# Optimization experiments

Measured on AMD Instinct MI355X. Metric: run time of the kernel, lower is better.

The kernel has to match this reference:

```python
import jax, jax.numpy as jnp
import numpy as np

IN_FEATURES = 4096
OUT_FEATURES = 4096
GROUP_SIZE = 128
N_GROUPS = IN_FEATURES // GROUP_SIZE
N_LEVELS = 16
SCALE = float(np.sqrt(GROUP_SIZE))


def setup_inputs() -> dict:
    key = jax.random.key(0)
    k_x, k_idx, k_cb, k_norm, k_rot = jax.random.split(key, 5)
    x = jax.random.normal(k_x, (4, 2048, IN_FEATURES), dtype=jnp.float32)
    # packed 4-bit indices: each uint8 byte holds two 4-bit codes (stored as int32 here)
    indices_packed = jax.random.randint(k_idx, (OUT_FEATURES, IN_FEATURES // 2), 0, 256, dtype=jnp.int32)
    codebook = jax.random.normal(k_cb, (N_LEVELS,), dtype=jnp.float32)
    weight_norms = jax.random.uniform(k_norm, (OUT_FEATURES, N_GROUPS), dtype=jnp.float32) + 0.5
    # per-group random orthogonal rotations (QR of gaussian), matching generate_rotation_matrix semantics
    g = jax.random.normal(k_rot, (N_GROUPS, GROUP_SIZE, GROUP_SIZE), dtype=jnp.float32)
    q, _ = jnp.linalg.qr(g)
    rotations = q.astype(jnp.float32)
    return {"x": x, "indices_packed": indices_packed, "codebook": codebook,
            "weight_norms": weight_norms, "rotations": rotations}


def _unpack_4bit(packed):
    # packed: (N, K//2) -> (N, K); even columns from low nibble, odd from high nibble
    low = packed & 0xF
    high = (packed >> 4) & 0xF
    return jnp.stack([low, high], axis=-1).reshape(packed.shape[0], -1)


def reference(x, indices_packed, codebook, weight_norms, rotations):
    B, S, K = x.shape
    xf = x.reshape(-1, K).astype(jnp.float32)            # (T, K)
    T = xf.shape[0]
    # group-wise rotation: x_rot_g = x_g @ Pi_g.T
    xg = xf.reshape(T, N_GROUPS, GROUP_SIZE)             # (T, G, g)
    x_rot = jnp.einsum('tgk,gjk->tgj', xg, rotations)    # (T, G, g)
    # dequantized codes (before norm scaling)
    idx = _unpack_4bit(indices_packed)                    # (N, K)
    W = codebook[idx].reshape(OUT_FEATURES, N_GROUPS, GROUP_SIZE)  # (N, G, g)
    # out[t,n] = sum_g (x_rot[t,g,:] . W[n,g,:]) * norms[n,g] / scale
    out = jnp.einsum('tgj,ngj,ng->tn', x_rot, W, weight_norms / SCALE)
    return out.reshape(B, S, OUT_FEATURES).astype(x.dtype)
```

## Files before the change

### kernel.cpp

```cpp
#include <hip/hip_runtime.h>

typedef __attribute__((ext_vector_type(8))) __bf16 bf16x8;
typedef __attribute__((ext_vector_type(4))) float f32x4;
typedef __attribute__((ext_vector_type(4))) int i32x4;
typedef __attribute__((ext_vector_type(8))) unsigned short ushort8;

#define T_TOKENS 8192
#define K_DIM    4096
#define N_DIM    4096
#define NGRP     32
#define GS       128

__device__ __forceinline__ unsigned short f2bf(float f) {
  unsigned u = __builtin_bit_cast(unsigned, f);
  u += 0x7fffu + ((u >> 16) & 1u);
  return (unsigned short)(u >> 16);
}

__device__ __forceinline__ f32x4 mfma16(bf16x8 a, bf16x8 b, f32x4 c) {
  return __builtin_amdgcn_mfma_f32_16x16x32_bf16(a, b, c, 0, 0, 0);
}

__device__ __forceinline__ i32x4 mfma_i8(i32x4 a, i32x4 b, i32x4 c) {
  return __builtin_amdgcn_mfma_i32_16x16x64_i8(a, b, c, 0, 0, 0);
}

__device__ __forceinline__ void gload_lds16(const void* g, void* l) {
  __builtin_amdgcn_global_load_lds(
      (const __attribute__((address_space(1))) void*)g,
      (__attribute__((address_space(3))) void*)l, 16, 0, 0);
}

__device__ __forceinline__ int clamp127(int q) {
  return q > 127 ? 127 : (q < -127 ? -127 : q);
}

__global__ __launch_bounds__(256) void k_prep(const float* __restrict__ x,
                                              signed char* __restrict__ qx,
                                              float* __restrict__ sxf,
                                              const int* __restrict__ idxp,
                                              const float* __restrict__ cb,
                                              const float* __restrict__ norms,
                                              const float* __restrict__ rot,
                                              unsigned short* __restrict__ weff,
                                              int* __restrict__ swmax) {
  __shared__ unsigned short Rt[128][136];
  __shared__ unsigned short Wq[128][136];
  __shared__ float cbl[16];
  const int tid = threadIdx.x;

  if (blockIdx.x < 2048) {
    const int wid = blockIdx.x * 4 + (tid >> 6);
    const int l = tid & 63;
    const float* xr = x + (size_t)wid * K_DIM;
    float4 v[16];
    float am = 0.f;
    #pragma unroll
    for (int i = 0; i < 16; ++i) {
      v[i] = *reinterpret_cast<const float4*>(xr + (i * 64 + l) * 4);
      am = fmaxf(am, fmaxf(fmaxf(fabsf(v[i].x), fabsf(v[i].y)),
                           fmaxf(fabsf(v[i].z), fabsf(v[i].w))));
    }
    #pragma unroll
    for (int m = 1; m < 64; m <<= 1) am = fmaxf(am, __shfl_xor(am, m, 64));
    const float inv = am > 0.f ? 127.0f / am : 0.f;
    #pragma unroll
    for (int i = 0; i < 16; ++i) {
      int q0 = clamp127(__float2int_rn(v[i].x * inv));
      int q1 = clamp127(__float2int_rn(v[i].y * inv));
      int q2 = clamp127(__float2int_rn(v[i].z * inv));
      int q3 = clamp127(__float2int_rn(v[i].w * inv));
      unsigned d = (q0 & 255) | ((q1 & 255) << 8) | ((q2 & 255) << 16) |
                   ((unsigned)(q3 & 255) << 24);
      *reinterpret_cast<unsigned*>(qx + (size_t)wid * K_DIM + (size_t)(i * 64 + l) * 4) = d;
    }
    if (l == 0) sxf[wid] = am * (1.0f / 127.0f);
    return;
  }

  const int v = blockIdx.x - 2048;
  const int nt = v & 31;
  const int g  = v >> 5;
  if (tid < 16) cbl[tid] = cb[tid];

  {
    const int j = tid >> 1, kh = (tid & 1) * 64;
    const float* rp = rot + ((size_t)g * 128 + j) * 128 + kh;
    #pragma unroll
    for (int c = 0; c < 64; c += 4) {
      float4 vv = *reinterpret_cast<const float4*>(rp + c);
      Rt[kh + c + 0][j] = f2bf(vv.x);
      Rt[kh + c + 1][j] = f2bf(vv.y);
      Rt[kh + c + 2][j] = f2bf(vv.z);
      Rt[kh + c + 3][j] = f2bf(vv.w);
    }
  }
  __syncthreads();

  {
    const int nl = tid >> 1, hf = (tid & 1);
    const int* ip = idxp + ((size_t)(nt * 128 + nl)) * (K_DIM / 2) + g * 64 + hf * 32;
    #pragma unroll
    for (int c = 0; c < 32; c += 4) {
      int4 vv = *reinterpret_cast<const int4*>(ip + c);
      int va[4] = {vv.x, vv.y, vv.z, vv.w};
      #pragma unroll
      for (int q = 0; q < 4; ++q) {
        int b = va[q] & 0xFF;
        Wq[nl][hf * 64 + (c + q) * 2 + 0] = f2bf(cbl[b & 0xF]);
        Wq[nl][hf * 64 + (c + q) * 2 + 1] = f2bf(cbl[(b >> 4) & 0xF]);
      }
    }
  }
  __syncthreads();

  const int w = tid >> 6, l = tid & 63;
  const int rl = l & 15, hi = l >> 4;
  f32x4 acc[2][8] = {};
  #pragma unroll
  for (int ks = 0; ks < 4; ++ks) {
    bf16x8 a0 = *(const bf16x8*)&Wq[w * 32 +  0 + rl][ks * 32 + hi * 8];
    bf16x8 a1 = *(const bf16x8*)&Wq[w * 32 + 16 + rl][ks * 32 + hi * 8];
    #pragma unroll
    for (int nc = 0; nc < 8; ++nc) {
      bf16x8 bfr = *(const bf16x8*)&Rt[nc * 16 + rl][ks * 32 + hi * 8];
      acc[0][nc] = mfma16(a0, bfr, acc[0][nc]);
      acc[1][nc] = mfma16(a1, bfr, acc[1][nc]);
    }
  }

  const float inv_scale = 0.088388347648318447f;
  #pragma unroll
  for (int m = 0; m < 2; ++m) {
    const int r0 = nt * 128 + w * 32 + m * 16 + hi * 4;
    float nv[4];
    #pragma unroll
    for (int r = 0; r < 4; ++r) nv[r] = norms[(size_t)(r0 + r) * NGRP + g] * inv_scale;
    float rowmax[4] = {0.f, 0.f, 0.f, 0.f};
    #pragma unroll
    for (int nc = 0; nc < 8; ++nc) {
      #pragma unroll
      for (int r = 0; r < 4; ++r) {
        float wv = acc[m][nc][r] * nv[r];
        weff[(size_t)(r0 + r) * K_DIM + g * GS + nc * 16 + rl] = f2bf(wv);
        rowmax[r] = fmaxf(rowmax[r], fabsf(wv));
      }
    }
    #pragma unroll
    for (int r = 0; r < 4; ++r) {
      #pragma unroll
      for (int msk = 1; msk < 16; msk <<= 1)
        rowmax[r] = fmaxf(rowmax[r], __shfl_xor(rowmax[r], msk, 64));
      if (rl == 0) atomicMax(&swmax[r0 + r], __float_as_int(rowmax[r]));
    }
  }
}

__global__ __launch_bounds__(256) void k_wquant(const unsigned short* __restrict__ weff,
                                                const int* __restrict__ swmax,
                                                signed char* __restrict__ qw,
                                                float* __restrict__ swf) {
  const int n = blockIdx.x, t = threadIdx.x;
  const float am = __int_as_float(swmax[n]);
  const float inv = am > 0.f ? 127.0f / am : 0.f;
  const unsigned short* wr = weff + (size_t)n * K_DIM + t * 16;
  ushort8 u0 = *(const ushort8*)wr;
  ushort8 u1 = *(const ushort8*)(wr + 8);
  unsigned d[4];
  #pragma unroll
  for (int j = 0; j < 2; ++j) {
    ushort8 u = j ? u1 : u0;
    #pragma unroll
    for (int h = 0; h < 2; ++h) {
      int q0 = clamp127(__float2int_rn(__uint_as_float((unsigned)u[h * 4 + 0] << 16) * inv));
      int q1 = clamp127(__float2int_rn(__uint_as_float((unsigned)u[h * 4 + 1] << 16) * inv));
      int q2 = clamp127(__float2int_rn(__uint_as_float((unsigned)u[h * 4 + 2] << 16) * inv));
      int q3 = clamp127(__float2int_rn(__uint_as_float((unsigned)u[h * 4 + 3] << 16) * inv));
      d[j * 2 + h] = (q0 & 255) | ((q1 & 255) << 8) | ((q2 & 255) << 16) |
                     ((unsigned)(q3 & 255) << 24);
    }
  }
  *reinterpret_cast<int4*>(qw + (size_t)n * K_DIM + t * 16) =
      make_int4((int)d[0], (int)d[1], (int)d[2], (int)d[3]);
  if (t == 0) swf[n] = am * (1.0f / 127.0f);
}

#define VMW asm volatile("s_waitcnt vmcnt(4)" ::: "memory")
#define NOW ((void)0)
#define BAR asm volatile("s_barrier" ::: "memory")

#define STG(gbase, koff, ldsoff) do { \
    gload_lds16((gbase) + (size_t)(koff), &lds[(ldsoff) + dst0]); \
    gload_lds16((gbase) + (size_t)(koff) + (size_t)64 * K_DIM, \
                &lds[(ldsoff) + dst0 + 4096]); \
  } while (0)

#define RD_B(PAR) { \
    const int bb = 32768 + (PAR) * 16384 + (wc >> 1) * 8192 + ((wc & 1) * 64 + rl) * 64; \
    _Pragma("unroll") \
    for (int n = 0; n < 4; ++n) { \
      bfr[n][0] = *(const i32x4*)&lds[bb + n * 1024 + slot0]; \
      bfr[n][1] = *(const i32x4*)&lds[bb + n * 1024 + slot1]; \
    } \
  }

#define RD_A(PAR, MQ, S) { \
    const int ab = (PAR) * 16384 + wr * 8192 + ((MQ) * 32 + rl) * 64; \
    S##0 = *(const i32x4*)&lds[ab + slot0]; \
    S##1 = *(const i32x4*)&lds[ab + slot1]; \
    S##2 = *(const i32x4*)&lds[ab + 1024 + slot0]; \
    S##3 = *(const i32x4*)&lds[ab + 1024 + slot1]; \
  }

#define MFMAQ(MQ, S) { \
    _Pragma("unroll") \
    for (int n = 0; n < 4; ++n) { \
      acc[(MQ)*2][n]     = mfma_i8(S##1, bfr[n][1], \
                             mfma_i8(S##0, bfr[n][0], acc[(MQ)*2][n])); \
      acc[(MQ)*2 + 1][n] = mfma_i8(S##3, bfr[n][1], \
                             mfma_i8(S##2, bfr[n][0], acc[(MQ)*2 + 1][n])); \
    } \
  }

#define PHX(MQ, RDB_PAR, RDB, VM, STGS, RDN, S) { \
    if (RDB) { RD_B(RDB_PAR) } \
    STGS; \
    VM; \
    BAR; \
    RDN; \
    __builtin_amdgcn_s_setprio(1); \
    MFMAQ(MQ, S) \
    __builtin_amdgcn_s_setprio(0); \
    BAR; \
  }

__global__ __launch_bounds__(512) void k_gemm(const signed char* __restrict__ A,
                                              const signed char* __restrict__ Bw,
                                              const float* __restrict__ sxf,
                                              const float* __restrict__ swf,
                                              float* __restrict__ C) {
  __shared__ unsigned short lds[65536];
  const int tid = threadIdx.x;
  const int l = tid & 63, w = tid >> 6;
  const int wr = w >> 2, wc = w & 3;
  const int rl = l & 15, hi = l >> 4;

  const int bid = blockIdx.x;
  const int xcd = bid & 7, jj = bid >> 3;
  const int brow = ((xcd >> 1) * 8 + (jj >> 3)) * 256;
  const int bcol = ((xcd & 1) * 8 + (jj & 7)) * 256;

  const int row0 = tid >> 3;
  const int gc = ((tid & 7) ^ (row0 & 7)) * 16;
  const signed char* pa  = A  + (size_t)(brow + row0) * K_DIM + gc;
  const signed char* pa2 = pa + (size_t)128 * K_DIM;
  const signed char* pb  = Bw + (size_t)(bcol + row0) * K_DIM + gc;
  const signed char* pb2 = pb + (size_t)128 * K_DIM;
  const int dst0 = tid * 8;

  const int rb7 = rl & 7;
  const int slot0 = ((0 + hi) ^ rb7) << 3;
  const int slot1 = ((4 + hi) ^ rb7) << 3;

  i32x4 acc[8][4] = {};
  i32x4 bfr[4][2];
  i32x4 af0, af1, af2, af3;
  i32x4 ag0, ag1, ag2, ag3;

  STG(pb,  0,   32768);
  STG(pb2, 0,   32768 + 8192);
  STG(pa,  0,   0);
  STG(pa2, 0,   8192);
  STG(pb,  128, 32768 + 16384);
  STG(pb2, 128, 32768 + 16384 + 8192);
  asm volatile("s_waitcnt vmcnt(4)" ::: "memory");
  asm volatile("s_barrier" ::: "memory");
  RD_A(0, 0, af)

  for (int it = 0; it < 16; ++it) {
    const int k0  = it * 256;
    const int kA1 = k0 + 128;
    const int kN0 = (k0 + 256) & (K_DIM - 1);
    const int kN1 = (k0 + 384) & (K_DIM - 1);
    PHX(0,   0,   1,  NOW, STG(pa,  kA1, 16384),              RD_A(0, 1, ag), af)
    PHX(1,   0,   0,  NOW, STG(pa2, kA1, 16384 + 8192),       RD_A(0, 2, af), ag)
    PHX(2,   0,   0,  NOW, STG(pb,  kN0, 32768),              RD_A(0, 3, ag), af)
    PHX(3,   0,   0,  VMW, STG(pb2, kN0, 32768 + 8192),       RD_A(1, 0, af), ag)
    PHX(0,   1,   1,  NOW, STG(pa,  kN0, 0),                  RD_A(1, 1, ag), af)
    PHX(1,   1,   0,  NOW, STG(pa2, kN0, 8192),               RD_A(1, 2, af), ag)
    PHX(2,   1,   0,  NOW, STG(pb,  kN1, 32768 + 16384),      RD_A(1, 3, ag), af)
    PHX(3,   1,   0,  VMW, STG(pb2, kN1, 32768 + 16384 + 8192), RD_A(0, 0, af), ag)
  }

  float swv[4];
  #pragma unroll
  for (int n = 0; n < 4; ++n) swv[n] = swf[bcol + wc * 64 + n * 16 + rl];
  #pragma unroll
  for (int m = 0; m < 8; ++m) {
    const int row = brow + wr * 128 + m * 16 + hi * 4;
    float sxr[4];
    #pragma unroll
    for (int r = 0; r < 4; ++r) sxr[r] = sxf[row + r];
    #pragma unroll
    for (int n = 0; n < 4; ++n) {
      const int col = bcol + wc * 64 + n * 16 + rl;
      #pragma unroll
      for (int r = 0; r < 4; ++r)
        C[(size_t)(row + r) * N_DIM + col] = (float)acc[m][n][r] * sxr[r] * swv[n];
    }
  }
}

extern "C" void kernel_launch(void* const* d_in, const int* in_sizes, int n_in,
                              void* d_out, int out_size, void* d_ws, size_t ws_size,
                              hipStream_t stream) {
  const float* x     = (const float*)d_in[0];
  const int*   idxp  = (const int*)d_in[1];
  const float* cb    = (const float*)d_in[2];
  const float* norms = (const float*)d_in[3];
  const float* rot   = (const float*)d_in[4];
  float* out = (float*)d_out;

  unsigned short* weff = (unsigned short*)d_ws;
  signed char* qw  = (signed char*)d_ws + 33554432;
  signed char* qx  = (signed char*)d_ws + 50331648;
  float* sxf   = (float*)((char*)d_ws + 83886080);
  int*   swmax = (int*)((char*)d_ws + 83918848);
  float* swf   = (float*)((char*)d_ws + 83935232);

  hipMemsetAsync(swmax, 0, 16384, stream);
  k_prep<<<3072, 256, 0, stream>>>(x, qx, sxf, idxp, cb, norms, rot, weff, swmax);
  k_wquant<<<4096, 256, 0, stream>>>(weff, swmax, qw, swf);
  k_gemm<<<512, 512, 0, stream>>>(qx, qw, sxf, swf, out);
}
```

Baseline: 207.4 us.

## Shrink int8 GEMM tile to 128x128 with 256-thread blocks and simpler phases

The int8 MFMA GEMM drops from 256x256 tiles with 8 waves to 128x128 tiles with 4 waves per block, launching 2048 blocks instead of 512. LDS use halves to 64 KB. The phase macro is simplified: the ping-pong A-fragment prefetch across phases is removed, and A fragments are now read at the start of each phase. The goal is better occupancy and load balance across CUs, at the cost of more global traffic per FLOP (less reuse) and less LDS-read/MFMA overlap within a phase.

```diff
diff --git a/kernel.cpp b/kernel.cpp
--- a/kernel.cpp
+++ b/kernel.cpp
@@ -191,12 +191,12 @@
 
 #define STG(gbase, koff, ldsoff) do { \
     gload_lds16((gbase) + (size_t)(koff), &lds[(ldsoff) + dst0]); \
-    gload_lds16((gbase) + (size_t)(koff) + (size_t)64 * K_DIM, \
-                &lds[(ldsoff) + dst0 + 4096]); \
+    gload_lds16((gbase) + (size_t)(koff) + (size_t)32 * K_DIM, \
+                &lds[(ldsoff) + dst0 + 2048]); \
   } while (0)
 
 #define RD_B(PAR) { \
-    const int bb = 32768 + (PAR) * 16384 + (wc >> 1) * 8192 + ((wc & 1) * 64 + rl) * 64; \
+    const int bb = 16384 + (PAR) * 8192 + (wc * 64 + rl) * 64; \
     _Pragma("unroll") \
     for (int n = 0; n < 4; ++n) { \
       bfr[n][0] = *(const i32x4*)&lds[bb + n * 1024 + slot0]; \
@@ -204,100 +204,90 @@
     } \
   }
 
-#define RD_A(PAR, MQ, S) { \
-    const int ab = (PAR) * 16384 + wr * 8192 + ((MQ) * 32 + rl) * 64; \
-    S##0 = *(const i32x4*)&lds[ab + slot0]; \
-    S##1 = *(const i32x4*)&lds[ab + slot1]; \
-    S##2 = *(const i32x4*)&lds[ab + 1024 + slot0]; \
-    S##3 = *(const i32x4*)&lds[ab + 1024 + slot1]; \
-  }
-
-#define MFMAQ(MQ, S) { \
+#define RD_A(PAR, MQ) { \
+    const int ab = (PAR) * 8192 + (wr * 64 + (MQ) * 16 + rl) * 64; \
+    af0 = *(const i32x4*)&lds[ab + slot0]; \
+    af1 = *(const i32x4*)&lds[ab + slot1]; \
+  }
+
+#define PHASE(MQ, PAR, RDB, TAIL, STGS) { \
+    if (RDB) { RD_B(PAR) } \
+    RD_A(PAR, MQ) \
+    STGS; \
+    BAR; \
+    __builtin_amdgcn_s_setprio(1); \
     _Pragma("unroll") \
     for (int n = 0; n < 4; ++n) { \
-      acc[(MQ)*2][n]     = mfma_i8(S##1, bfr[n][1], \
-                             mfma_i8(S##0, bfr[n][0], acc[(MQ)*2][n])); \
-      acc[(MQ)*2 + 1][n] = mfma_i8(S##3, bfr[n][1], \
-                             mfma_i8(S##2, bfr[n][0], acc[(MQ)*2 + 1][n])); \
+      acc[MQ][n] = mfma_i8(af1, bfr[n][1], \
+                     mfma_i8(af0, bfr[n][0], acc[MQ][n])); \
     } \
-  }
-
-#define PHX(MQ, RDB_PAR, RDB, VM, STGS, RDN, S) { \
-    if (RDB) { RD_B(RDB_PAR) } \
-    STGS; \
-    VM; \
+    __builtin_amdgcn_s_setprio(0); \
+    TAIL; \
     BAR; \
-    RDN; \
-    __builtin_amdgcn_s_setprio(1); \
-    MFMAQ(MQ, S) \
-    __builtin_amdgcn_s_setprio(0); \
-    BAR; \
-  }
-
-__global__ __launch_bounds__(512) void k_gemm(const signed char* __restrict__ A,
+  }
+
+__global__ __launch_bounds__(256) void k_gemm(const signed char* __restrict__ A,
                                               const signed char* __restrict__ Bw,
                                               const float* __restrict__ sxf,
                                               const float* __restrict__ swf,
                                               float* __restrict__ C) {
-  __shared__ unsigned short lds[65536];
+  __shared__ unsigned short lds[32768];
   const int tid = threadIdx.x;
   const int l = tid & 63, w = tid >> 6;
-  const int wr = w >> 2, wc = w & 3;
+  const int wr = w >> 1, wc = w & 1;
   const int rl = l & 15, hi = l >> 4;
 
   const int bid = blockIdx.x;
   const int xcd = bid & 7, jj = bid >> 3;
-  const int brow = ((xcd >> 1) * 8 + (jj >> 3)) * 256;
-  const int bcol = ((xcd & 1) * 8 + (jj & 7)) * 256;
+  const int brow = ((xcd >> 1) * 16 + (jj >> 4)) * 128;
+  const int bcol = ((xcd & 1) * 16 + (jj & 15)) * 128;
 
   const int row0 = tid >> 3;
   const int gc = ((tid & 7) ^ (row0 & 7)) * 16;
   const signed char* pa  = A  + (size_t)(brow + row0) * K_DIM + gc;
-  const signed char* pa2 = pa + (size_t)128 * K_DIM;
+  const signed char* pa2 = pa + (size_t)64 * K_DIM;
   const signed char* pb  = Bw + (size_t)(bcol + row0) * K_DIM + gc;
-  const signed char* pb2 = pb + (size_t)128 * K_DIM;
+  const signed char* pb2 = pb + (size_t)64 * K_DIM;
   const int dst0 = tid * 8;
 
   const int rb7 = rl & 7;
   const int slot0 = ((0 + hi) ^ rb7) << 3;
   const int slot1 = ((4 + hi) ^ rb7) << 3;
 
-  i32x4 acc[8][4] = {};
+  i32x4 acc[4][4] = {};
   i32x4 bfr[4][2];
-  i32x4 af0, af1, af2, af3;
-  i32x4 ag0, ag1, ag2, ag3;
-
-  STG(pb,  0,   32768);
-  STG(pb2, 0,   32768 + 8192);
+  i32x4 af0, af1;
+
+  STG(pb,  0,   16384);
+  STG(pb2, 0,   16384 + 4096);
   STG(pa,  0,   0);
-  STG(pa2, 0,   8192);
-  STG(pb,  128, 32768 + 16384);
-  STG(pb2, 128, 32768 + 16384 + 8192);
+  STG(pa2, 0,   4096);
+  STG(pb,  128, 24576);
+  STG(pb2, 128, 24576 + 4096);
   asm volatile("s_waitcnt vmcnt(4)" ::: "memory");
   asm volatile("s_barrier" ::: "memory");
-  RD_A(0, 0, af)
 
   for (int it = 0; it < 16; ++it) {
     const int k0  = it * 256;
     const int kA1 = k0 + 128;
     const int kN0 = (k0 + 256) & (K_DIM - 1);
     const int kN1 = (k0 + 384) & (K_DIM - 1);
-    PHX(0,   0,   1,  NOW, STG(pa,  kA1, 16384),              RD_A(0, 1, ag), af)
-    PHX(1,   0,   0,  NOW, STG(pa2, kA1, 16384 + 8192),       RD_A(0, 2, af), ag)
-    PHX(2,   0,   0,  NOW, STG(pb,  kN0, 32768),              RD_A(0, 3, ag), af)
-    PHX(3,   0,   0,  VMW, STG(pb2, kN0, 32768 + 8192),       RD_A(1, 0, af), ag)
-    PHX(0,   1,   1,  NOW, STG(pa,  kN0, 0),                  RD_A(1, 1, ag), af)
-    PHX(1,   1,   0,  NOW, STG(pa2, kN0, 8192),               RD_A(1, 2, af), ag)
-    PHX(2,   1,   0,  NOW, STG(pb,  kN1, 32768 + 16384),      RD_A(1, 3, ag), af)
-    PHX(3,   1,   0,  VMW, STG(pb2, kN1, 32768 + 16384 + 8192), RD_A(0, 0, af), ag)
+    PHASE(0, 0,  1, NOW, STG(pa,  kA1, 8192))
+    PHASE(1, 0,  0, NOW, STG(pa2, kA1, 8192 + 4096))
+    PHASE(2, 0,  0, NOW, STG(pb,  kN0, 16384))
+    PHASE(3, 0,  0, VMW, STG(pb2, kN0, 16384 + 4096))
+    PHASE(0, 1,  1, NOW, STG(pa,  kN0, 0))
+    PHASE(1, 1,  0, NOW, STG(pa2, kN0, 4096))
+    PHASE(2, 1,  0, NOW, STG(pb,  kN1, 24576))
+    PHASE(3, 1,  0, VMW, STG(pb2, kN1, 24576 + 4096))
   }
 
   float swv[4];
   #pragma unroll
   for (int n = 0; n < 4; ++n) swv[n] = swf[bcol + wc * 64 + n * 16 + rl];
   #pragma unroll
-  for (int m = 0; m < 8; ++m) {
-    const int row = brow + wr * 128 + m * 16 + hi * 4;
+  for (int m = 0; m < 4; ++m) {
+    const int row = brow + wr * 64 + m * 16 + hi * 4;
     float sxr[4];
     #pragma unroll
     for (int r = 0; r < 4; ++r) sxr[r] = sxf[row + r];
@@ -331,5 +321,5 @@
   hipMemsetAsync(swmax, 0, 16384, stream);
   k_prep<<<3072, 256, 0, stream>>>(x, qx, sxf, idxp, cb, norms, rot, weff, swmax);
   k_wquant<<<4096, 256, 0, stream>>>(weff, swmax, qw, swf);
-  k_gemm<<<512, 512, 0, stream>>>(qx, qw, sxf, swf, out);
-}
+  k_gemm<<<2048, 256, 0, stream>>>(qx, qw, sxf, swf, out);
+}
```

Measured after the change: 212.4 us. +2.4%, slower.

## Load A operand directly from global into registers, stage only B in LDS

Applied to the files above, without the earlier changes.

The int8 GEMM main loop no longer stages the activation (A) tile through LDS. Each wave now loads its A fragments straight from global memory into registers, and only the weight (B) tile is double-buffered in LDS. This halves LDS usage and reduces the barriers per K-step from two per phase to one per half-iteration, with a vmcnt(12) wait before each barrier. In exchange, A rows are read redundantly by the four waves that share a row block, which adds global/L2 traffic. The A loads are also narrower, more scattered accesses whose latency has to be hidden by the MFMA work.

```diff
diff --git a/kernel.cpp b/kernel.cpp
--- a/kernel.cpp
+++ b/kernel.cpp
@@ -185,18 +185,18 @@
   if (t == 0) swf[n] = am * (1.0f / 127.0f);
 }
 
-#define VMW asm volatile("s_waitcnt vmcnt(4)" ::: "memory")
-#define NOW ((void)0)
-#define BAR asm volatile("s_barrier" ::: "memory")
-
-#define STG(gbase, koff, ldsoff) do { \
-    gload_lds16((gbase) + (size_t)(koff), &lds[(ldsoff) + dst0]); \
-    gload_lds16((gbase) + (size_t)(koff) + (size_t)64 * K_DIM, \
-                &lds[(ldsoff) + dst0 + 4096]); \
+#define VMW12 asm volatile("s_waitcnt vmcnt(12)" ::: "memory")
+#define BAR   asm volatile("s_barrier" ::: "memory")
+
+#define STG_B(kb, roff) do { \
+    gload_lds16(pb  + (size_t)(unsigned)(kb), &lds[(roff) + dst0]); \
+    gload_lds16(pb  + (size_t)(unsigned)(kb) + (size_t)64 * K_DIM, &lds[(roff) + dst0 + 4096]); \
+    gload_lds16(pb2 + (size_t)(unsigned)(kb), &lds[(roff) + dst0 + 8192]); \
+    gload_lds16(pb2 + (size_t)(unsigned)(kb) + (size_t)64 * K_DIM, &lds[(roff) + dst0 + 12288]); \
   } while (0)
 
-#define RD_B(PAR) { \
-    const int bb = 32768 + (PAR) * 16384 + (wc >> 1) * 8192 + ((wc & 1) * 64 + rl) * 64; \
+#define RD_B(roff) { \
+    const int bb = (roff) + (wc >> 1) * 8192 + ((wc & 1) * 64 + rl) * 64; \
     _Pragma("unroll") \
     for (int n = 0; n < 4; ++n) { \
       bfr[n][0] = *(const i32x4*)&lds[bb + n * 1024 + slot0]; \
@@ -204,15 +204,16 @@
     } \
   }
 
-#define RD_A(PAR, MQ, S) { \
-    const int ab = (PAR) * 16384 + wr * 8192 + ((MQ) * 32 + rl) * 64; \
-    S##0 = *(const i32x4*)&lds[ab + slot0]; \
-    S##1 = *(const i32x4*)&lds[ab + slot1]; \
-    S##2 = *(const i32x4*)&lds[ab + 1024 + slot0]; \
-    S##3 = *(const i32x4*)&lds[ab + 1024 + slot1]; \
+#define ALD(kb, MQ, S) { \
+    const signed char* p_ = paw + (size_t)(unsigned)(kb) + (size_t)((MQ) * 32) * K_DIM; \
+    S##0 = *(const i32x4*)(p_); \
+    S##1 = *(const i32x4*)(p_ + 64); \
+    S##2 = *(const i32x4*)(p_ + (size_t)16 * K_DIM); \
+    S##3 = *(const i32x4*)(p_ + (size_t)16 * K_DIM + 64); \
   }
 
 #define MFMAQ(MQ, S) { \
+    __builtin_amdgcn_s_setprio(1); \
     _Pragma("unroll") \
     for (int n = 0; n < 4; ++n) { \
       acc[(MQ)*2][n]     = mfma_i8(S##1, bfr[n][1], \
@@ -220,18 +221,7 @@
       acc[(MQ)*2 + 1][n] = mfma_i8(S##3, bfr[n][1], \
                              mfma_i8(S##2, bfr[n][0], acc[(MQ)*2 + 1][n])); \
     } \
-  }
-
-#define PHX(MQ, RDB_PAR, RDB, VM, STGS, RDN, S) { \
-    if (RDB) { RD_B(RDB_PAR) } \
-    STGS; \
-    VM; \
-    BAR; \
-    RDN; \
-    __builtin_amdgcn_s_setprio(1); \
-    MFMAQ(MQ, S) \
     __builtin_amdgcn_s_setprio(0); \
-    BAR; \
   }
 
 __global__ __launch_bounds__(512) void k_gemm(const signed char* __restrict__ A,
@@ -239,7 +229,7 @@
                                               const float* __restrict__ sxf,
                                               const float* __restrict__ swf,
                                               float* __restrict__ C) {
-  __shared__ unsigned short lds[65536];
+  __shared__ unsigned short lds[32768];
   const int tid = threadIdx.x;
   const int l = tid & 63, w = tid >> 6;
   const int wr = w >> 2, wc = w & 3;
@@ -252,8 +242,6 @@
 
   const int row0 = tid >> 3;
   const int gc = ((tid & 7) ^ (row0 & 7)) * 16;
-  const signed char* pa  = A  + (size_t)(brow + row0) * K_DIM + gc;
-  const signed char* pa2 = pa + (size_t)128 * K_DIM;
   const signed char* pb  = Bw + (size_t)(bcol + row0) * K_DIM + gc;
   const signed char* pb2 = pb + (size_t)128 * K_DIM;
   const int dst0 = tid * 8;
@@ -261,35 +249,38 @@
   const int rb7 = rl & 7;
   const int slot0 = ((0 + hi) ^ rb7) << 3;
   const int slot1 = ((4 + hi) ^ rb7) << 3;
+
+  const signed char* paw = A + (size_t)(brow + wr * 128 + rl) * K_DIM + hi * 16;
 
   i32x4 acc[8][4] = {};
   i32x4 bfr[4][2];
   i32x4 af0, af1, af2, af3;
   i32x4 ag0, ag1, ag2, ag3;
 
-  STG(pb,  0,   32768);
-  STG(pb2, 0,   32768 + 8192);
-  STG(pa,  0,   0);
-  STG(pa2, 0,   8192);
-  STG(pb,  128, 32768 + 16384);
-  STG(pb2, 128, 32768 + 16384 + 8192);
-  asm volatile("s_waitcnt vmcnt(4)" ::: "memory");
-  asm volatile("s_barrier" ::: "memory");
-  RD_A(0, 0, af)
+  STG_B(0, 0);
+  asm volatile("s_waitcnt vmcnt(0)" ::: "memory");
+  BAR;
+  RD_B(0)
+  ALD(0, 0, af)
 
   for (int it = 0; it < 16; ++it) {
-    const int k0  = it * 256;
-    const int kA1 = k0 + 128;
-    const int kN0 = (k0 + 256) & (K_DIM - 1);
-    const int kN1 = (k0 + 384) & (K_DIM - 1);
-    PHX(0,   0,   1,  NOW, STG(pa,  kA1, 16384),              RD_A(0, 1, ag), af)
-    PHX(1,   0,   0,  NOW, STG(pa2, kA1, 16384 + 8192),       RD_A(0, 2, af), ag)
-    PHX(2,   0,   0,  NOW, STG(pb,  kN0, 32768),              RD_A(0, 3, ag), af)
-    PHX(3,   0,   0,  VMW, STG(pb2, kN0, 32768 + 8192),       RD_A(1, 0, af), ag)
-    PHX(0,   1,   1,  NOW, STG(pa,  kN0, 0),                  RD_A(1, 1, ag), af)
-    PHX(1,   1,   0,  NOW, STG(pa2, kN0, 8192),               RD_A(1, 2, af), ag)
-    PHX(2,   1,   0,  NOW, STG(pb,  kN1, 32768 + 16384),      RD_A(1, 3, ag), af)
-    PHX(3,   1,   0,  VMW, STG(pb2, kN1, 32768 + 16384 + 8192), RD_A(0, 0, af), ag)
+    const int kb0 = it * 256;
+    const int kb1 = kb0 + 128;
+    const int kb2 = (kb0 + 256) & (K_DIM - 1);
+    ALD(kb0, 1, ag) MFMAQ(0, af)
+    STG_B(kb1, 16384);
+    ALD(kb0, 2, af) MFMAQ(1, ag)
+    ALD(kb0, 3, ag) MFMAQ(2, af)
+    ALD(kb1, 0, af) MFMAQ(3, ag)
+    VMW12; BAR;
+    RD_B(16384)
+    ALD(kb1, 1, ag) MFMAQ(0, af)
+    STG_B(kb2, 0);
+    ALD(kb1, 2, af) MFMAQ(1, ag)
+    ALD(kb1, 3, ag) MFMAQ(2, af)
+    ALD(kb2, 0, af) MFMAQ(3, ag)
+    VMW12; BAR;
+    RD_B(0)
   }
 
   float swv[4];
```

Result: slower. 343.1 us (+65.4%).
